# Performance work log

Hardware: AMD Instinct MI355X
Metric: run time of the kernel (lower is better)

The kernel has to match this reference:

```python
import jax, jax.numpy as jnp
import numpy as np

B, N, K, IN_CH = 512, 64, 16, 6   # graphs, nodes per graph, knn, input features
EPS = 1e-5


def _w(key, shape, fan_in):
    return jax.random.normal(key, shape, jnp.float32) / np.sqrt(fan_in)


def setup_inputs() -> dict:
    key = jax.random.key(0)
    ks = jax.random.split(key, 16)
    f32 = jnp.float32
    inp = {
        "x": jax.random.normal(ks[0], (B * N, IN_CH), f32),
        "batch": (jnp.arange(B * N, dtype=jnp.int32) // N).astype(jnp.int32),
        # input projection 6 -> 64
        "w_in": _w(ks[1], (IN_CH, 64), IN_CH), "g_in": jnp.ones(64, f32), "b_in": jnp.zeros(64, f32),
        # ec1: SharedMLP([128, 64, 64])
        "w1a": _w(ks[2], (128, 64), 128), "g1a": jnp.ones(64, f32), "b1a": jnp.zeros(64, f32),
        "w1b": _w(ks[3], (64, 64), 64),   "g1b": jnp.ones(64, f32), "b1b": jnp.zeros(64, f32),
        # ec2: SharedMLP([128, 128, 128])
        "w2a": _w(ks[4], (128, 128), 128), "g2a": jnp.ones(128, f32), "b2a": jnp.zeros(128, f32),
        "w2b": _w(ks[5], (128, 128), 128), "g2b": jnp.ones(128, f32), "b2b": jnp.zeros(128, f32),
        # ec3: SharedMLP([256, 256, 256])
        "w3a": _w(ks[6], (256, 256), 256), "g3a": jnp.ones(256, f32), "b3a": jnp.zeros(256, f32),
        "w3b": _w(ks[7], (256, 256), 256), "g3b": jnp.ones(256, f32), "b3b": jnp.zeros(256, f32),
        # classifier head (dropout is identity in eval mode)
        "wc1": _w(ks[8], (896, 512), 896), "gc1": jnp.ones(512, f32), "bc1": jnp.zeros(512, f32),
        "wc2": _w(ks[9], (512, 256), 512), "gc2": jnp.ones(256, f32), "bc2": jnp.zeros(256, f32),
        "wc3": _w(ks[10], (256, 2), 256),  "bc3": jnp.zeros(2, f32),
    }
    return inp


def bn(h, g, b):
    # training-mode BatchNorm1d over all leading (node/edge) dims, biased var
    ax = tuple(range(h.ndim - 1))
    m = h.mean(ax)
    v = h.var(ax)
    return g * (h - m) * jax.lax.rsqrt(v + EPS) + b


def lrelu(h):
    return jax.nn.leaky_relu(h, 0.2)


def knn(x):
    # x: [B,N,C]; per-graph squared-Euclidean kNN (excluding self)
    sq = jnp.sum(x * x, -1)
    d = sq[:, :, None] - 2.0 * jnp.einsum('bnc,bmc->bnm', x, x) + sq[:, None, :]
    _, idx = jax.lax.top_k(-d, K + 1)  # K+1 smallest distances
    return idx[:, :, 1:]               # drop self -> [B,N,K]


def edge_conv(x, w1, g1, b1, w2, g2, b2):
    # Dynamic EdgeConv, aggr='max'. Edge (src=centre c, dst=neighbour n):
    # target x_i = x_n, message = MLP(cat[x_i, x_j - x_i]) with x_j = x_c.
    idx = knn(x)                                     # [B,N,K]
    xn = jax.vmap(lambda xb, ib: xb[ib])(x, idx)     # [B,N,K,C] neighbours
    xc = x[:, :, None, :]                            # centres broadcast
    feat = jnp.concatenate([xn, xc - xn], -1)        # [B,N,K,2C]
    h = lrelu(bn(feat @ w1, g1, b1))
    h = lrelu(bn(h @ w2, g2, b2))                    # [B,N,K,Cout]
    C = h.shape[-1]

    def scatter_max(ib, hb):  # per-graph max-scatter to destination nodes
        out = jnp.full((N, C), -jnp.inf, hb.dtype)
        return out.at[ib.reshape(-1)].max(hb.reshape(-1, C))

    res = jax.vmap(scatter_max)(idx, h)
    return jnp.where(jnp.isneginf(res), 0.0, res)    # nodes w/o in-edges -> 0


def reference(x, batch, w_in, g_in, b_in,
              w1a, g1a, b1a, w1b, g1b, b1b,
              w2a, g2a, b2a, w2b, g2b, b2b,
              w3a, g3a, b3a, w3b, g3b, b3b,
              wc1, gc1, bc1, wc2, gc2, bc2, wc3, bc3):
    # batch == arange(B*N)//N (equal-size graphs), encoded by the [B,N] reshape
    h0 = lrelu(bn(x @ w_in, g_in, b_in)).reshape(B, N, 64)
    h1 = edge_conv(h0, w1a, g1a, b1a, w1b, g1b, b1b)   # [B,N,64]
    h2 = edge_conv(h1, w2a, g2a, b2a, w2b, g2b, b2b)   # [B,N,128]
    h3 = edge_conv(h2, w3a, g3a, b3a, w3b, g3b, b3b)   # [B,N,256]
    h = jnp.concatenate([h1, h2, h3], -1)              # [B,N,448]
    pooled = jnp.concatenate([h.mean(1), h.max(1)], -1)  # [B,896]
    z = lrelu(bn(pooled @ wc1, gc1, bc1))
    z = lrelu(bn(z @ wc2, gc2, bc2))
    return z @ wc3 + bc3                               # [B,2] logits
```

## Files before the change

### kernel.cpp

```cpp
#include <hip/hip_runtime.h>
#include <hip/hip_fp16.h>
#include <math.h>

#define BB 512
#define NN 64
#define KNB 16
#define NPTS (BB*NN)
#define NEDGE (BB*NN*KNB)
#define EPSV 1e-5f

typedef __attribute__((ext_vector_type(8))) _Float16 f16x8;
typedef __attribute__((ext_vector_type(4))) _Float16 f16x4;
typedef __attribute__((ext_vector_type(4))) float f32x4;

__device__ __forceinline__ float lrelu(float x){ return fmaxf(x, 0.2f*x); }
__device__ __forceinline__ unsigned encf(float f){
    unsigned u = __float_as_uint(f);
    return (u & 0x80000000u) ? ~u : (u | 0x80000000u);
}
__device__ __forceinline__ float decf(unsigned e){
    unsigned u = (e & 0x80000000u) ? (e ^ 0x80000000u) : ~e;
    return __uint_as_float(u);
}
#define ENC_NEGINF 0x007FFFFFu

__device__ __forceinline__ void split2h(float v, _Float16& h, _Float16& m){
    h = (_Float16)v;
    float r = v - (float)h;
    m = (_Float16)(r * 2048.0f);
}

__global__ void k_input(const float* __restrict__ x, const float* __restrict__ w,
                        float* __restrict__ h0){
    __shared__ float wls[6*64];
    int t = threadIdx.x;
    for (int i = t; i < 6*64; i += 256) wls[i] = w[i];
    __syncthreads();
    int row = blockIdx.x*256 + t;
    float xv[6];
#pragma unroll
    for (int k = 0; k < 6; k++) xv[k] = x[row*6 + k];
#pragma unroll 8
    for (int c = 0; c < 64; c++){
        float acc = 0.f;
#pragma unroll
        for (int k = 0; k < 6; k++) acc += xv[k]*wls[k*64 + c];
        h0[(size_t)row*64 + c] = acc;
    }
}

__global__ void k_colstats_part(const float* __restrict__ h,
                                float* __restrict__ pS, float* __restrict__ pQ){
    int t = threadIdx.x;
    int c = t & 63;
    int g = t >> 6;
    int p = blockIdx.x*4 + g;
    const int rpb = NPTS/256;
    int r0 = p*rpb;
    float s = 0.f, q = 0.f;
    for (int r = r0; r < r0 + rpb; r++){
        float v = h[(size_t)r*64 + c];
        s += v; q += v*v;
    }
    pS[c*256 + p] = s;
    pQ[c*256 + p] = q;
}

__global__ void k_bnfin_part(const float* __restrict__ pS, const float* __restrict__ pQ,
                             const float* __restrict__ g, const float* __restrict__ b,
                             float* __restrict__ cA, float* __restrict__ cB,
                             int P, float invM){
    int c = threadIdx.x;
    const float* ps = pS + (size_t)c*P;
    const float* pq = pQ + (size_t)c*P;
    float s = 0.f, q = 0.f;
    for (int p = 0; p < P; p += 4){
        float4 vs = *(const float4*)(ps + p);
        float4 vq = *(const float4*)(pq + p);
        s += vs.x + vs.y + vs.z + vs.w;
        q += vq.x + vq.y + vq.z + vq.w;
    }
    float m = s*invM;
    float v = q*invM - m*m;
    v = v < 0.f ? 0.f : v;
    float a = g[c]*rsqrtf(v + EPSV);
    cA[c] = a;
    cB[c] = b[c] - m*a;
}

__global__ void k_bnfin(const float* gs, const float* gq, const float* g,
                        const float* b, float* cA, float* cB, int C, float invM){
    int c = blockIdx.x*blockDim.x + threadIdx.x;
    if (c < C){
        float m = gs[c]*invM;
        float v = gq[c]*invM - m*m;
        v = v < 0.f ? 0.f : v;
        float a = g[c]*rsqrtf(v + EPSV);
        cA[c] = a;
        cB[c] = b[c] - m*a;
    }
}

__global__ void k_apply(float* h, const float* __restrict__ cA,
                        const float* __restrict__ cB, int C, int total){
    int i = blockIdx.x*256 + threadIdx.x;
    if (i < total){
        int c = i & (C-1);
        h[i] = lrelu(cA[c]*h[i] + cB[c]);
    }
}

template<int C>
__global__ void k_knn(const float* __restrict__ x, int* __restrict__ idxg){
    const int CP = C + 4;
    __shared__ __align__(16) float xls[64*CP];
    __shared__ float sq[64];
    __shared__ __align__(16) float dls[64*64];
    int t = threadIdx.x, b = blockIdx.x;
    const float* xb = x + (size_t)b*64*C;
    for (int i = t; i < 64*C; i += 256){
        int n = i / C, c = i & (C-1);
        xls[n*CP + c] = xb[i];
    }
    __syncthreads();
    if (t < 64){
        float s = 0.f;
        for (int c = 0; c < C; c += 4){
            float4 v = *(const float4*)&xls[t*CP + c];
            s += v.x*v.x + v.y*v.y + v.z*v.z + v.w*v.w;
        }
        sq[t] = s;
    }
    __syncthreads();
    {
        int n  = t >> 2;
        int m0 = (t & 3)*16;
        float acc[16];
#pragma unroll
        for (int i = 0; i < 16; i++) acc[i] = 0.f;
        const float* an = &xls[n*CP];
        const float* bm = &xls[m0*CP];
        for (int c = 0; c < C; c += 4){
            float4 a = *(const float4*)(an + c);
#pragma unroll
            for (int i = 0; i < 16; i++){
                float4 bv = *(const float4*)(bm + i*CP + c);
                acc[i] += a.x*bv.x + a.y*bv.y + a.z*bv.z + a.w*bv.w;
            }
        }
        float sn = sq[n];
#pragma unroll
        for (int i4 = 0; i4 < 16; i4 += 4){
            float4 dv;
            dv.x = sn - 2.0f*acc[i4+0] + sq[m0+i4+0];
            dv.y = sn - 2.0f*acc[i4+1] + sq[m0+i4+1];
            dv.z = sn - 2.0f*acc[i4+2] + sq[m0+i4+2];
            dv.w = sn - 2.0f*acc[i4+3] + sq[m0+i4+3];
            *(float4*)&dls[n*64 + m0 + i4] = dv;
        }
    }
    __syncthreads();
    int lane = t & 63, w = t >> 6;
    for (int pr = 0; pr < 16; pr += 4){
        int n0 = w*16 + pr;
        unsigned long long c0 = (((unsigned long long)encf(dls[(n0+0)*64 + lane])) << 32) | (unsigned)lane;
        unsigned long long c1 = (((unsigned long long)encf(dls[(n0+1)*64 + lane])) << 32) | (unsigned)lane;
        unsigned long long c2 = (((unsigned long long)encf(dls[(n0+2)*64 + lane])) << 32) | (unsigned)lane;
        unsigned long long c3 = (((unsigned long long)encf(dls[(n0+3)*64 + lane])) << 32) | (unsigned)lane;
#pragma unroll
        for (int k = 2; k <= 64; k <<= 1){
#pragma unroll
            for (int j = k >> 1; j > 0; j >>= 1){
                bool keepmin = ((lane & j) == 0) == ((lane & k) == 0);
                unsigned long long o0 = __shfl_xor(c0, j, 64);
                unsigned long long o1 = __shfl_xor(c1, j, 64);
                unsigned long long o2 = __shfl_xor(c2, j, 64);
                unsigned long long o3 = __shfl_xor(c3, j, 64);
                c0 = keepmin ? (c0 < o0 ? c0 : o0) : (c0 < o0 ? o0 : c0);
                c1 = keepmin ? (c1 < o1 ? c1 : o1) : (c1 < o1 ? o1 : c1);
                c2 = keepmin ? (c2 < o2 ? c2 : o2) : (c2 < o2 ? o2 : c2);
                c3 = keepmin ? (c3 < o3 ? c3 : o3) : (c3 < o3 ? o3 : c3);
            }
        }
        if (lane >= 1 && lane <= KNB){
            int base = b*1024 + n0*16 + lane - 1;
            idxg[base]      = (int)(c0 & 0xffffffffu);
            idxg[base + 16] = (int)(c1 & 0xffffffffu);
            idxg[base + 32] = (int)(c2 & 0xffffffffu);
            idxg[base + 48] = (int)(c3 & 0xffffffffu);
        }
    }
}

__global__ void k_wprep_all(const float* __restrict__ w1a, const float* __restrict__ w2a,
                            const float* __restrict__ w3a,
                            _Float16* __restrict__ w1bh, _Float16* __restrict__ w1bm,
                            _Float16* __restrict__ w1dh, _Float16* __restrict__ w1dm,
                            _Float16* __restrict__ w2bh, _Float16* __restrict__ w2bm,
                            _Float16* __restrict__ w2dh, _Float16* __restrict__ w2dm,
                            _Float16* __restrict__ w3bh, _Float16* __restrict__ w3dh){
    int blk = blockIdx.x, t = threadIdx.x;
    if (blk < 16){
        const int CIN = 64, CMID = 64;
        int i = blk*256 + t;
        int k = i / CMID, c = i - k*CMID;
        float wb = w1a[(size_t)(CIN + k)*CMID + c];
        float wd = w1a[(size_t)k*CMID + c] - wb;
        size_t o = (size_t)c*CIN + k;
        _Float16 h, m;
        split2h(wb, h, m); w1bh[o] = h; w1bm[o] = m;
        split2h(wd, h, m); w1dh[o] = h; w1dm[o] = m;
    } else if (blk < 48){
        const int CIN = 64, CMID = 128;
        int i = (blk - 16)*256 + t;
        int k = i / CMID, c = i - k*CMID;
        float wb = w2a[(size_t)(CIN + k)*CMID + c];
        float wd = w2a[(size_t)k*CMID + c] - wb;
        size_t o = (size_t)c*CIN + k;
        _Float16 h, m;
        split2h(wb, h, m); w2bh[o] = h; w2bm[o] = m;
        split2h(wd, h, m); w2dh[o] = h; w2dm[o] = m;
    } else {
        const int CIN = 128, CMID = 256;
        int i = (blk - 48)*256 + t;
        int k = i / CMID, c = i - k*CMID;
        float wb = w3a[(size_t)(CIN + k)*CMID + c];
        float wd = w3a[(size_t)k*CMID + c] - wb;
        size_t o = (size_t)c*CIN + k;
        w3bh[o] = (_Float16)wb;
        w3dh[o] = (_Float16)wd;
    }
}

template<int CIN, int CMID>
__global__ __launch_bounds__(256)
void k_mm1x(const float* __restrict__ x,
            const _Float16* __restrict__ wbh, const _Float16* __restrict__ wbm,
            const _Float16* __restrict__ wdh, const _Float16* __restrict__ wdm,
            float* __restrict__ P, float* __restrict__ Q){
    int t = threadIdx.x, b = blockIdx.x;
    int lane = t & 63, w = t >> 6;
    int lrow = lane & 15, lk = lane >> 4;
    const int KT = CIN/32;
    f16x8 ah[KT], am[KT];
    {
        const float* xr = x + ((size_t)b*64 + w*16 + lrow)*CIN;
#pragma unroll
        for (int kt = 0; kt < KT; kt++){
            union { f16x8 v; _Float16 u[8]; } H, M;
#pragma unroll
            for (int j = 0; j < 8; j++)
                split2h(xr[kt*32 + lk*8 + j], H.u[j], M.u[j]);
            ah[kt] = H.v; am[kt] = M.v;
        }
    }
#pragma unroll
    for (int ct = 0; ct < CMID/16; ct++){
        int col = ct*16 + lrow;
        f32x4 aPM = {0,0,0,0}, aPC = {0,0,0,0};
        f32x4 aQM = {0,0,0,0}, aQC = {0,0,0,0};
#pragma unroll
        for (int kt = 0; kt < KT; kt++){
            size_t bo = (size_t)col*CIN + kt*32 + lk*8;
            f16x8 bbh = *(const f16x8*)(wbh + bo);
            f16x8 bbm = *(const f16x8*)(wbm + bo);
            f16x8 bdh = *(const f16x8*)(wdh + bo);
            f16x8 bdm = *(const f16x8*)(wdm + bo);
            aPM = __builtin_amdgcn_mfma_f32_16x16x32_f16(ah[kt], bbh, aPM, 0, 0, 0);
            aPC = __builtin_amdgcn_mfma_f32_16x16x32_f16(ah[kt], bbm, aPC, 0, 0, 0);
            aPC = __builtin_amdgcn_mfma_f32_16x16x32_f16(am[kt], bbh, aPC, 0, 0, 0);
            aQM = __builtin_amdgcn_mfma_f32_16x16x32_f16(ah[kt], bdh, aQM, 0, 0, 0);
            aQC = __builtin_amdgcn_mfma_f32_16x16x32_f16(ah[kt], bdm, aQC, 0, 0, 0);
            aQC = __builtin_amdgcn_mfma_f32_16x16x32_f16(am[kt], bdh, aQC, 0, 0, 0);
        }
#pragma unroll
        for (int u = 0; u < 4; u++){
            size_t o = ((size_t)b*64 + w*16 + lk*4 + u)*CMID + col;
            P[o] = aPM[u] + aPC[u]*(1.0f/2048.0f);
            Q[o] = aQM[u] + aQC[u]*(1.0f/2048.0f);
        }
    }
}

template<int CIN, int CMID>
__global__ __launch_bounds__(256)
void k_mm1xh(const float* __restrict__ x,
             const _Float16* __restrict__ wbh, const _Float16* __restrict__ wdh,
             _Float16* __restrict__ P, _Float16* __restrict__ Q){
    int t = threadIdx.x, b = blockIdx.x;
    int lane = t & 63, w = t >> 6;
    int lrow = lane & 15, lk = lane >> 4;
    const int KT = CIN/32;
    f16x8 ah[KT];
    {
        const float* xr = x + ((size_t)b*64 + w*16 + lrow)*CIN;
#pragma unroll
        for (int kt = 0; kt < KT; kt++){
            union { f16x8 v; _Float16 u[8]; } H;
#pragma unroll
            for (int j = 0; j < 8; j++)
                H.u[j] = (_Float16)xr[kt*32 + lk*8 + j];
            ah[kt] = H.v;
        }
    }
#pragma unroll
    for (int ct = 0; ct < CMID/16; ct++){
        int col = ct*16 + lrow;
        f32x4 aP = {0,0,0,0}, aQ = {0,0,0,0};
#pragma unroll
        for (int kt = 0; kt < KT; kt++){
            size_t bo = (size_t)col*CIN + kt*32 + lk*8;
            f16x8 bbh = *(const f16x8*)(wbh + bo);
            f16x8 bdh = *(const f16x8*)(wdh + bo);
            aP = __builtin_amdgcn_mfma_f32_16x16x32_f16(ah[kt], bbh, aP, 0, 0, 0);
            aQ = __builtin_amdgcn_mfma_f32_16x16x32_f16(ah[kt], bdh, aQ, 0, 0, 0);
        }
#pragma unroll
        for (int u = 0; u < 4; u++){
            size_t o = ((size_t)b*64 + w*16 + lk*4 + u)*CMID + col;
            P[o] = (_Float16)aP[u];
            Q[o] = (_Float16)aQ[u];
        }
    }
}

template<int CMID>
__global__ void k_stats1p(const float* __restrict__ P, const float* __restrict__ Q,
                          const int* __restrict__ idxg,
                          float* __restrict__ pS, float* __restrict__ pQ){
    int t = threadIdx.x, b = blockIdx.x;
    const int NG = 256/CMID;
    const int PT = 512*NG;
    int c = t & (CMID-1);
    int g = t / CMID;
    int epg = 1024/NG;
    const float* Pb = P + (size_t)b*64*CMID;
    const float* Qb = Q + (size_t)b*64*CMID;
    const int* ib = idxg + b*1024;
    float s = 0.f, q = 0.f;
    for (int e = g*epg; e < (g+1)*epg; e++){
        int n = e >> 4;
        int j = ib[e];
        float v = Pb[n*CMID + c] + Qb[j*CMID + c];
        s += v; q += v*v;
    }
    int p = b*NG + g;
    pS[(size_t)c*PT + p] = s;
    pQ[(size_t)c*PT + p] = q;
}

__global__ void k_stats1h(const _Float16* __restrict__ P, const _Float16* __restrict__ Q,
                          const int* __restrict__ idxg,
                          float* __restrict__ pS, float* __restrict__ pQ){
    __shared__ int ils[1024];
    int t = threadIdx.x, b = blockIdx.x;
    for (int i = t; i < 1024; i += 256) ils[i] = idxg[b*1024 + i];
    __syncthreads();
    const _Float16* Pb = P + (size_t)b*64*256;
    const _Float16* Qb = Q + (size_t)b*64*256;
    float s = 0.f, q = 0.f;
    for (int n = 0; n < 64; n++){
        float p = (float)Pb[n*256 + t];
#pragma unroll 4
        for (int k = 0; k < 16; k++){
            int j = ils[n*16 + k];
            float v = p + (float)Qb[j*256 + t];
            s += v; q += v*v;
        }
    }
    pS[(size_t)t*512 + b] = s;
    pQ[(size_t)t*512 + b] = q;
}

template<int CMID, int COUT, int NSET>
__global__ __launch_bounds__(256, 3)
void k_mm2s(const float* __restrict__ P, const float* __restrict__ Q,
            const int* __restrict__ idxg,
            const float* __restrict__ cA1, const float* __restrict__ cB1,
            const float* __restrict__ w2, const float* __restrict__ g2,
            unsigned* __restrict__ outenc,
            float* __restrict__ pS, float* __restrict__ pQ){
    const int AS = CMID + 8;
    const int NCOL = 64*NSET;
    const int NM = CMID/32;
    __shared__ __align__(16) _Float16 act_h[32*AS];
    __shared__ __align__(16) _Float16 act_m[32*AS];
    __shared__ unsigned maxtab[NCOL*65];
    __shared__ __align__(4) unsigned char ils8[1024];
    int t = threadIdx.x, b = blockIdx.x, cc = blockIdx.y;
    int lane = t & 63, w = t >> 6;
    int lrow = lane & 15, lk = lane >> 4;

    for (int i = t; i < 1024; i += 256) ils8[i] = (unsigned char)idxg[b*1024 + i];
    for (int i = t; i < NCOL*65; i += 256) maxtab[i] = ENC_NEGINF;

    int kq  = (t*4) & (CMID-1);
    int le0 = (t*4) / CMID;
    int PH  = (le0*NM) >> 4;
    float4 caq = *(const float4*)(cA1 + kq);
    float4 cbq = *(const float4*)(cB1 + kq);

    const int KT = CMID/32;
    f16x8 bh[NSET][KT], bm[NSET][KT];
    float sg[NSET];
    int ccBase = cc*NCOL;
#pragma unroll
    for (int s = 0; s < NSET; s++){
        int ncol = ccBase + s*64 + w*16 + lrow;
#pragma unroll
        for (int kt = 0; kt < KT; kt++){
            union { f16x8 v; _Float16 u[8]; } uh, um;
#pragma unroll
            for (int j = 0; j < 8; j++){
                int k = kt*32 + lk*8 + j;
                split2h(w2[(size_t)k*COUT + ncol], uh.u[j], um.u[j]);
            }
            bh[s][kt] = uh.v; bm[s][kt] = um.v;
        }
        sg[s] = (g2[ncol] < 0.0f) ? -1.0f : 1.0f;
    }
    float ss[NSET], qq[NSET];
#pragma unroll
    for (int s = 0; s < NSET; s++){ ss[s] = 0.f; qq[s] = 0.f; }
    const float* Pb = P + (size_t)b*64*CMID;
    const float* Qb = Q + (size_t)b*64*CMID;
    __syncthreads();

    unsigned jw;
    if (NM == 4) jw = *(const unsigned*)&ils8[le0*4];
    else         jw = *(const unsigned short*)&ils8[le0*2];
    float4 pv = *(const float4*)(Pb + PH*CMID + kq);
    float4 qvr[NM];
#pragma unroll
    for (int m = 0; m < NM; m++)
        qvr[m] = *(const float4*)(Qb + (size_t)((jw >> (8*m)) & 0xffu)*CMID + kq);

    for (int ch = 0; ch < 32; ch++){
#pragma unroll
        for (int m = 0; m < NM; m++){
            int le = le0*NM + m;
            float4 qv = qvr[m];
            float v0 = lrelu(caq.x*(pv.x + qv.x) + cbq.x);
            float v1 = lrelu(caq.y*(pv.y + qv.y) + cbq.y);
            float v2 = lrelu(caq.z*(pv.z + qv.z) + cbq.z);
            float v3 = lrelu(caq.w*(pv.w + qv.w) + cbq.w);
            union { f16x4 v; _Float16 u[4]; } hh, mm;
            split2h(v0, hh.u[0], mm.u[0]);
            split2h(v1, hh.u[1], mm.u[1]);
            split2h(v2, hh.u[2], mm.u[2]);
            split2h(v3, hh.u[3], mm.u[3]);
            *(f16x4*)&act_h[le*AS + kq] = hh.v;
            *(f16x4*)&act_m[le*AS + kq] = mm.v;
        }
        __syncthreads();

        if (ch < 31){
            if (NM == 4) jw = *(const unsigned*)&ils8[(ch+1)*32 + le0*4];
            else         jw = *(const unsigned short*)&ils8[(ch+1)*32 + le0*2];
            pv = *(const float4*)(Pb + (2*(ch+1) + PH)*CMID + kq);
#pragma unroll
            for (int m = 0; m < NM; m++)
                qvr[m] = *(const float4*)(Qb + (size_t)((jw >> (8*m)) & 0xffu)*CMID + kq);
        }
        int jj[2][4];
#pragma unroll
        for (int r = 0; r < 2; r++){
            unsigned wrd = *(const unsigned*)&ils8[ch*32 + r*16 + lk*4];
#pragma unroll
            for (int u = 0; u < 4; u++)
                jj[r][u] = (int)((wrd >> (8*u)) & 0xffu);
        }

        f32x4 accM[2][NSET], accC[2][NSET];
#pragma unroll
        for (int r = 0; r < 2; r++)
#pragma unroll
            for (int s = 0; s < NSET; s++){
                accM[r][s] = {0.f,0.f,0.f,0.f};
                accC[r][s] = {0.f,0.f,0.f,0.f};
            }
#pragma unroll
        for (int kt = 0; kt < KT; kt++){
            int ko = kt*32 + lk*8;
#pragma unroll
            for (int r = 0; r < 2; r++){
                f16x8 ah = *(const f16x8*)&act_h[(r*16 + lrow)*AS + ko];
                f16x8 am = *(const f16x8*)&act_m[(r*16 + lrow)*AS + ko];
#pragma unroll
                for (int s = 0; s < NSET; s++){
                    accM[r][s] = __builtin_amdgcn_mfma_f32_16x16x32_f16(ah, bh[s][kt], accM[r][s], 0, 0, 0);
                    accC[r][s] = __builtin_amdgcn_mfma_f32_16x16x32_f16(ah, bm[s][kt], accC[r][s], 0, 0, 0);
                    accC[r][s] = __builtin_amdgcn_mfma_f32_16x16x32_f16(am, bh[s][kt], accC[r][s], 0, 0, 0);
                }
            }
        }
#pragma unroll
        for (int r = 0; r < 2; r++){
#pragma unroll
            for (int s = 0; s < NSET; s++){
#pragma unroll
                for (int u = 0; u < 4; u++){
                    float v = accM[r][s][u] + accC[r][s][u]*(1.0f/2048.0f);
                    ss[s] += v; qq[s] += v*v;
                    int colL = s*64 + w*16 + lrow;
                    atomicMax(&maxtab[colL*65 + jj[r][u]], encf(sg[s]*v));
                }
            }
        }
        __syncthreads();
    }
#pragma unroll
    for (int s = 0; s < NSET; s++){
        ss[s] += __shfl_xor(ss[s], 16, 64); ss[s] += __shfl_xor(ss[s], 32, 64);
        qq[s] += __shfl_xor(qq[s], 16, 64); qq[s] += __shfl_xor(qq[s], 32, 64);
        if (lane < 16){
            pS[(size_t)(ccBase + s*64 + w*16 + lane)*512 + b] = ss[s];
            pQ[(size_t)(ccBase + s*64 + w*16 + lane)*512 + b] = qq[s];
        }
    }
    for (int i = t; i < 64*NCOL; i += 256){
        int colL = i % NCOL, j = i / NCOL;
        outenc[((size_t)b*64 + j)*COUT + ccBase + colL] = maxtab[colL*65 + j];
    }
}

template<int CMID, int COUT, int NSET>
__global__ __launch_bounds__(256, 3)
void k_mm2xh(const _Float16* __restrict__ P, const _Float16* __restrict__ Q,
             const int* __restrict__ idxg,
             const float* __restrict__ cA1, const float* __restrict__ cB1,
             const float* __restrict__ w2, const float* __restrict__ g2,
             unsigned* __restrict__ outenc,
             float* __restrict__ pS, float* __restrict__ pQ){
    const int AS = CMID + 8;
    const int NCOL = 64*NSET;
    const int NM = CMID/64;
    __shared__ __align__(16) _Float16 act[32*AS];
    __shared__ unsigned maxtab[NCOL*65];
    __shared__ __align__(4) unsigned char ils8[1024];
    int t = threadIdx.x, b = blockIdx.x, cc = blockIdx.y;
    int lane = t & 63, w = t >> 6;
    int lrow = lane & 15, lk = lane >> 4;

    for (int i = t; i < 1024; i += 256) ils8[i] = (unsigned char)idxg[b*1024 + i];
    for (int i = t; i < NCOL*65; i += 256) maxtab[i] = ENC_NEGINF;

    int kq  = (t*8) & (CMID-1);
    int le0 = (t*8) / CMID;
    int PH  = (le0*NM) >> 4;
    union { f16x8 v; _Float16 u[8]; } cah, cbh;
#pragma unroll
    for (int j = 0; j < 8; j++){
        cah.u[j] = (_Float16)cA1[kq + j];
        cbh.u[j] = (_Float16)cB1[kq + j];
    }

    const int KT = CMID/32;
    f16x8 breg[NSET][KT];
    float sg[NSET];
    int ccBase = cc*NCOL;
#pragma unroll
    for (int s = 0; s < NSET; s++){
        int ncol = ccBase + s*64 + w*16 + lrow;
#pragma unroll
        for (int kt = 0; kt < KT; kt++){
            union { f16x8 v; _Float16 u[8]; } bu;
#pragma unroll
            for (int j = 0; j < 8; j++){
                int k = kt*32 + lk*8 + j;
                bu.u[j] = (_Float16)w2[(size_t)k*COUT + ncol];
            }
            breg[s][kt] = bu.v;
        }
        sg[s] = (g2[ncol] < 0.0f) ? -1.0f : 1.0f;
    }
    float ss[NSET], qq[NSET];
#pragma unroll
    for (int s = 0; s < NSET; s++){ ss[s] = 0.f; qq[s] = 0.f; }
    const _Float16* Pb = P + (size_t)b*64*CMID;
    const _Float16* Qb = Q + (size_t)b*64*CMID;
    __syncthreads();

    unsigned jw = *(const unsigned*)&ils8[le0*4];
    f16x8 pv = *(const f16x8*)(Pb + (size_t)PH*CMID + kq);
    f16x8 qvr[NM];
#pragma unroll
    for (int m = 0; m < NM; m++)
        qvr[m] = *(const f16x8*)(Qb + (size_t)((jw >> (8*m)) & 0xffu)*CMID + kq);

    for (int ch = 0; ch < 32; ch++){
#pragma unroll
        for (int m = 0; m < NM; m++){
            int le = le0*NM + m;
            f16x8 v = cah.v*(pv + qvr[m]) + cbh.v;
            f16x8 vm = v * (_Float16)0.2f;
#if __has_builtin(__builtin_elementwise_max)
            *(f16x8*)&act[le*AS + kq] = __builtin_elementwise_max(v, vm);
#else
            union { f16x8 x; _Float16 e8[8]; } V, M, R;
            V.x = v; M.x = vm;
#pragma unroll
            for (int u = 0; u < 8; u++)
                R.e8[u] = (V.e8[u] > (_Float16)0.0f) ? V.e8[u] : M.e8[u];
            *(f16x8*)&act[le*AS + kq] = R.x;
#endif
        }
        __syncthreads();

        if (ch < 31){
            jw = *(const unsigned*)&ils8[(ch+1)*32 + le0*4];
            pv = *(const f16x8*)(Pb + (size_t)(2*(ch+1) + PH)*CMID + kq);
#pragma unroll
            for (int m = 0; m < NM; m++)
                qvr[m] = *(const f16x8*)(Qb + (size_t)((jw >> (8*m)) & 0xffu)*CMID + kq);
        }
        int jj[2][4];
#pragma unroll
        for (int r = 0; r < 2; r++){
            unsigned wrd = *(const unsigned*)&ils8[ch*32 + r*16 + lk*4];
#pragma unroll
            for (int u = 0; u < 4; u++)
                jj[r][u] = (int)((wrd >> (8*u)) & 0xffu);
        }

        f32x4 acc[2][NSET];
#pragma unroll
        for (int r = 0; r < 2; r++)
#pragma unroll
            for (int s = 0; s < NSET; s++) acc[r][s] = {0.f,0.f,0.f,0.f};
#pragma unroll
        for (int kt = 0; kt < KT; kt++){
            int ko = kt*32 + lk*8;
#pragma unroll
            for (int r = 0; r < 2; r++){
                f16x8 a = *(const f16x8*)&act[(r*16 + lrow)*AS + ko];
#pragma unroll
                for (int s = 0; s < NSET; s++)
                    acc[r][s] = __builtin_amdgcn_mfma_f32_16x16x32_f16(a, breg[s][kt], acc[r][s], 0, 0, 0);
            }
        }
#pragma unroll
        for (int r = 0; r < 2; r++){
#pragma unroll
            for (int s = 0; s < NSET; s++){
#pragma unroll
                for (int u = 0; u < 4; u++){
                    float v = acc[r][s][u];
                    ss[s] += v; qq[s] += v*v;
                    int colL = s*64 + w*16 + lrow;
                    atomicMax(&maxtab[colL*65 + jj[r][u]], encf(sg[s]*v));
                }
            }
        }
        __syncthreads();
    }
#pragma unroll
    for (int s = 0; s < NSET; s++){
        ss[s] += __shfl_xor(ss[s], 16, 64); ss[s] += __shfl_xor(ss[s], 32, 64);
        qq[s] += __shfl_xor(qq[s], 16, 64); qq[s] += __shfl_xor(qq[s], 32, 64);
        if (lane < 16){
            pS[(size_t)(ccBase + s*64 + w*16 + lane)*512 + b] = ss[s];
            pQ[(size_t)(ccBase + s*64 + w*16 + lane)*512 + b] = qq[s];
        }
    }
    for (int i = t; i < 64*NCOL; i += 256){
        int colL = i % NCOL, j = i / NCOL;
        outenc[((size_t)b*64 + j)*COUT + ccBase + colL] = maxtab[colL*65 + j];
    }
}

__global__ void k_final_ec(unsigned* __restrict__ buf, const float* __restrict__ cA,
                           const float* __restrict__ cB, const float* __restrict__ g,
                           int C, int total){
    int i = blockIdx.x*256 + threadIdx.x;
    if (i >= total) return;
    int c = i & (C-1);
    unsigned e = buf[i];
    float r;
    if (e == ENC_NEGINF) r = 0.0f;
    else {
        float s = (g[c] < 0.0f) ? -1.0f : 1.0f;
        float v = s*decf(e);
        r = lrelu(cA[c]*v + cB[c]);
    }
    ((float*)buf)[i] = r;
}

__global__ void k_pool(const float* __restrict__ h1, const float* __restrict__ h2,
                       const unsigned* __restrict__ h3e,
                       const float* __restrict__ cA3, const float* __restrict__ cB3,
                       const float* __restrict__ g3, float* __restrict__ pooled){
    int t = threadIdx.x, b = blockIdx.x;
    for (int c = t; c < 448; c += 256){
        float s = 0.f, mx = -INFINITY;
        if (c < 192){
            const float* src; int C, cl;
            if (c < 64){ src = h1; C = 64;  cl = c; }
            else { src = h2; C = 128; cl = c - 64; }
            const float* p = src + (size_t)b*64*C + cl;
            for (int n = 0; n < 64; n++){
                float v = p[(size_t)n*C];
                s += v; mx = fmaxf(mx, v);
            }
        } else {
            int cl = c - 192;
            float ca = cA3[cl], cb = cB3[cl];
            float sgn = (g3[cl] < 0.0f) ? -1.0f : 1.0f;
            const unsigned* p = h3e + (size_t)b*64*256 + cl;
            for (int n = 0; n < 64; n++){
                unsigned e = p[(size_t)n*256];
                float v;
                if (e == ENC_NEGINF) v = 0.0f;
                else v = lrelu(ca*(sgn*decf(e)) + cb);
                s += v; mx = fmaxf(mx, v);
            }
        }
        pooled[b*896 + c] = s*(1.0f/64.0f);
        pooled[b*896 + 448 + c] = mx;
    }
}

__global__ void k_fc1(const float* __restrict__ pooled, const float* __restrict__ w,
                      float* __restrict__ z, float* gs, float* gq){
    int r = blockIdx.x;
    int co = blockIdx.y*256 + threadIdx.x;
    const float* pr = pooled + r*896;
    float acc = 0.f;
    for (int k = 0; k < 896; k++) acc += pr[k]*w[(size_t)k*512 + co];
    z[(size_t)r*512 + co] = acc;
    atomicAdd(&gs[co], acc);
    atomicAdd(&gq[co], acc*acc);
}

__global__ void k_fc2(const float* __restrict__ z1, const float* __restrict__ cA,
                      const float* __restrict__ cB, const float* __restrict__ w,
                      float* __restrict__ z2, float* gs, float* gq){
    int r = blockIdx.x;
    int co = threadIdx.x;
    const float* zr = z1 + (size_t)r*512;
    float acc = 0.f;
    for (int k = 0; k < 512; k++){
        float v = lrelu(cA[k]*zr[k] + cB[k]);
        acc += v*w[(size_t)k*256 + co];
    }
    z2[(size_t)r*256 + co] = acc;
    atomicAdd(&gs[co], acc);
    atomicAdd(&gq[co], acc*acc);
}

__global__ void k_fc3(const float* __restrict__ z2, const float* __restrict__ cA,
                      const float* __restrict__ cB, const float* __restrict__ w,
                      const float* __restrict__ bias, float* __restrict__ out){
    int r = blockIdx.x*256 + threadIdx.x;
    const float* zr = z2 + (size_t)r*256;
    float a0 = 0.f, a1 = 0.f;
    for (int k = 0; k < 256; k++){
        float v = lrelu(cA[k]*zr[k] + cB[k]);
        a0 += v*w[k*2 + 0];
        a1 += v*w[k*2 + 1];
    }
    out[r*2 + 0] = a0 + bias[0];
    out[r*2 + 1] = a1 + bias[1];
}

extern "C" void kernel_launch(void* const* d_in, const int* in_sizes, int n_in,
                              void* d_out, int out_size, void* d_ws, size_t ws_size,
                              hipStream_t stream){
    const float* x    = (const float*)d_in[0];
    const float* w_in = (const float*)d_in[2];
    const float* g_in = (const float*)d_in[3];
    const float* b_in = (const float*)d_in[4];
    const float* w1a  = (const float*)d_in[5];
    const float* g1a  = (const float*)d_in[6];
    const float* b1a  = (const float*)d_in[7];
    const float* w1b  = (const float*)d_in[8];
    const float* g1b  = (const float*)d_in[9];
    const float* b1b  = (const float*)d_in[10];
    const float* w2a  = (const float*)d_in[11];
    const float* g2a  = (const float*)d_in[12];
    const float* b2a  = (const float*)d_in[13];
    const float* w2b  = (const float*)d_in[14];
    const float* g2b  = (const float*)d_in[15];
    const float* b2b  = (const float*)d_in[16];
    const float* w3a  = (const float*)d_in[17];
    const float* g3a  = (const float*)d_in[18];
    const float* b3a  = (const float*)d_in[19];
    const float* w3b  = (const float*)d_in[20];
    const float* g3b  = (const float*)d_in[21];
    const float* b3b  = (const float*)d_in[22];
    const float* wc1  = (const float*)d_in[23];
    const float* gc1  = (const float*)d_in[24];
    const float* bc1  = (const float*)d_in[25];
    const float* wc2  = (const float*)d_in[26];
    const float* gc2  = (const float*)d_in[27];
    const float* bc2  = (const float*)d_in[28];
    const float* wc3  = (const float*)d_in[29];
    const float* bc3  = (const float*)d_in[30];

    char* ws = (char*)d_ws;
    size_t off = 0;
    auto alloc = [&](size_t bytes){
        size_t o = off; off = (off + bytes + 255) & ~(size_t)255; return o;
    };
    float* h0     = (float*)(ws + alloc((size_t)NPTS*64*4));
    float* h1     = (float*)(ws + alloc((size_t)NPTS*64*4));
    float* h2     = (float*)(ws + alloc((size_t)NPTS*128*4));
    float* h3     = (float*)(ws + alloc((size_t)NPTS*256*4));
    float* P      = (float*)(ws + alloc((size_t)NPTS*256*4));
    float* Q      = (float*)(ws + alloc((size_t)NPTS*256*4));
    int*   idx    = (int*)  (ws + alloc((size_t)NPTS*16*4));
    float* pooled = (float*)(ws + alloc((size_t)512*896*4));
    float* z1     = (float*)(ws + alloc((size_t)512*512*4));
    float* z2     = (float*)(ws + alloc((size_t)512*256*4));
    float* pS     = (float*)(ws + alloc((size_t)131072*4));
    float* pQ     = (float*)(ws + alloc((size_t)131072*4));
    float* stats  = (float*)(ws + alloc((size_t)2048*4));
    float* coefs  = (float*)(ws + alloc((size_t)3456*4));
    _Float16* wsp = (_Float16*)(ws + alloc((size_t)114688*2));

    _Float16 *w1bh = wsp,          *w1bm = wsp+4096,
             *w1dh = wsp+8192,     *w1dm = wsp+12288;
    _Float16 *w2bh = wsp+16384,    *w2bm = wsp+24576,
             *w2dh = wsp+32768,    *w2dm = wsp+40960;
    _Float16 *w3bh = wsp+49152,    *w3dh = wsp+81920;

    float *f1s  = stats,       *f1q  = stats+512;
    float *f2s  = stats+1024,  *f2q  = stats+1280;
    float *cA0   = coefs,      *cB0   = coefs+64;
    float *cA1a  = coefs+128,  *cB1a  = coefs+192;
    float *cA1b  = coefs+256,  *cB1b  = coefs+320;
    float *cA2a  = coefs+384,  *cB2a  = coefs+512;
    float *cA2b  = coefs+640,  *cB2b  = coefs+768;
    float *cA3a  = coefs+896,  *cB3a  = coefs+1152;
    float *cA3b  = coefs+1408, *cB3b  = coefs+1664;
    float *cAf1  = coefs+1920, *cBf1  = coefs+2432;
    float *cAf2  = coefs+2944, *cBf2  = coefs+3200;

    (void)hipMemsetAsync(stats, 0, 2048*4, stream);

    k_wprep_all<<<176, 256, 0, stream>>>(w1a, w2a, w3a,
                                         w1bh, w1bm, w1dh, w1dm,
                                         w2bh, w2bm, w2dh, w2dm,
                                         w3bh, w3dh);

    k_input<<<NPTS/256, 256, 0, stream>>>(x, w_in, h0);
    k_colstats_part<<<64, 256, 0, stream>>>(h0, pS, pQ);
    k_bnfin_part<<<1, 64, 0, stream>>>(pS, pQ, g_in, b_in, cA0, cB0, 256, 1.0f/NPTS);
    k_apply<<<(NPTS*64)/256, 256, 0, stream>>>(h0, cA0, cB0, 64, NPTS*64);

    k_knn<64><<<BB, 256, 0, stream>>>(h0, idx);
    k_mm1x<64,64><<<BB, 256, 0, stream>>>(h0, w1bh, w1bm, w1dh, w1dm, P, Q);
    k_stats1p<64><<<BB, 256, 0, stream>>>(P, Q, idx, pS, pQ);
    k_bnfin_part<<<1, 64, 0, stream>>>(pS, pQ, g1a, b1a, cA1a, cB1a, 2048, 1.0f/NEDGE);
    k_mm2s<64,64,1><<<dim3(BB,1), 256, 0, stream>>>(P, Q, idx, cA1a, cB1a, w1b, g1b,
                                                    (unsigned*)h1, pS, pQ);
    k_bnfin_part<<<1, 64, 0, stream>>>(pS, pQ, g1b, b1b, cA1b, cB1b, 512, 1.0f/NEDGE);
    k_final_ec<<<(NPTS*64)/256, 256, 0, stream>>>((unsigned*)h1, cA1b, cB1b, g1b, 64, NPTS*64);

    k_knn<64><<<BB, 256, 0, stream>>>(h1, idx);
    k_mm1x<64,128><<<BB, 256, 0, stream>>>(h1, w2bh, w2bm, w2dh, w2dm, P, Q);
    k_stats1p<128><<<BB, 256, 0, stream>>>(P, Q, idx, pS, pQ);
    k_bnfin_part<<<1, 128, 0, stream>>>(pS, pQ, g2a, b2a, cA2a, cB2a, 1024, 1.0f/NEDGE);
    k_mm2s<128,128,2><<<dim3(BB,1), 256, 0, stream>>>(P, Q, idx, cA2a, cB2a, w2b, g2b,
                                                      (unsigned*)h2, pS, pQ);
    k_bnfin_part<<<1, 128, 0, stream>>>(pS, pQ, g2b, b2b, cA2b, cB2b, 512, 1.0f/NEDGE);
    k_final_ec<<<(NPTS*128)/256, 256, 0, stream>>>((unsigned*)h2, cA2b, cB2b, g2b, 128, NPTS*128);

    k_knn<128><<<BB, 256, 0, stream>>>(h2, idx);
    k_mm1xh<128,256><<<BB, 256, 0, stream>>>(h2, w3bh, w3dh, (_Float16*)P, (_Float16*)Q);
    k_stats1h<<<BB, 256, 0, stream>>>((_Float16*)P, (_Float16*)Q, idx, pS, pQ);
    k_bnfin_part<<<1, 256, 0, stream>>>(pS, pQ, g3a, b3a, cA3a, cB3a, 512, 1.0f/NEDGE);
    k_mm2xh<256,256,2><<<dim3(BB,2), 256, 0, stream>>>((_Float16*)P, (_Float16*)Q, idx,
                                                       cA3a, cB3a, w3b, g3b,
                                                       (unsigned*)h3, pS, pQ);
    k_bnfin_part<<<1, 256, 0, stream>>>(pS, pQ, g3b, b3b, cA3b, cB3b, 512, 1.0f/NEDGE);

    k_pool<<<BB, 256, 0, stream>>>(h1, h2, (const unsigned*)h3, cA3b, cB3b, g3b, pooled);
    k_fc1<<<dim3(512,2), 256, 0, stream>>>(pooled, wc1, z1, f1s, f1q);
    k_bnfin<<<2, 256, 0, stream>>>(f1s, f1q, gc1, bc1, cAf1, cBf1, 512, 1.0f/512);
    k_fc2<<<512, 256, 0, stream>>>(z1, cAf1, cBf1, wc2, z2, f2s, f2q);
    k_bnfin<<<1, 256, 0, stream>>>(f2s, f2q, gc2, bc2, cAf2, cBf2, 256, 1.0f/512);
    k_fc3<<<2, 256, 0, stream>>>(z2, cAf2, cBf2, wc3, bc3, (float*)d_out);

    (void)in_sizes; (void)n_in; (void)out_size; (void)ws_size;
}
```

Measured before the change: 1.139 ms.

## Fuse BN-apply and decode into consumers; fold edge stats into first matmul

Removes the standalone BN-apply and final edge-conv decode passes. Consumers (knn, first-layer matmul, pool) now apply the BN affine, leaky ReLU and max-encoding decode on the fly as they read. The per-edge BN statistics kernels are folded into the first edge-conv matmul: P and Q tiles are staged in shared memory and reduced using the neighbour indices. This cuts several launches and full-tensor global round trips, at the cost of repeated decode work in multiple consumers and higher LDS use per block.

```diff
diff --git a/kernel.cpp b/kernel.cpp
--- a/kernel.cpp
+++ b/kernel.cpp
@@ -23,6 +23,12 @@
     return __uint_as_float(u);
 }
 #define ENC_NEGINF 0x007FFFFFu
+
+__device__ __forceinline__ float dec_ec(unsigned e, float ca, float cb, float gv){
+    if (e == ENC_NEGINF) return 0.0f;
+    float s = (gv < 0.0f) ? -1.0f : 1.0f;
+    return lrelu(ca*(s*decf(e)) + cb);
+}
 
 __device__ __forceinline__ void split2h(float v, _Float16& h, _Float16& m){
     h = (_Float16)v;
@@ -101,26 +107,27 @@
     }
 }
 
-__global__ void k_apply(float* h, const float* __restrict__ cA,
-                        const float* __restrict__ cB, int C, int total){
-    int i = blockIdx.x*256 + threadIdx.x;
-    if (i < total){
-        int c = i & (C-1);
-        h[i] = lrelu(cA[c]*h[i] + cB[c]);
-    }
-}
-
-template<int C>
-__global__ void k_knn(const float* __restrict__ x, int* __restrict__ idxg){
+template<int C, int MODE>
+__global__ void k_knn(const void* __restrict__ xin, int* __restrict__ idxg,
+                      const float* __restrict__ cA, const float* __restrict__ cB,
+                      const float* __restrict__ g){
     const int CP = C + 4;
     __shared__ __align__(16) float xls[64*CP];
     __shared__ float sq[64];
     __shared__ __align__(16) float dls[64*64];
     int t = threadIdx.x, b = blockIdx.x;
-    const float* xb = x + (size_t)b*64*C;
-    for (int i = t; i < 64*C; i += 256){
-        int n = i / C, c = i & (C-1);
-        xls[n*CP + c] = xb[i];
+    if (MODE == 0){
+        const float* xb = (const float*)xin + (size_t)b*64*C;
+        for (int i = t; i < 64*C; i += 256){
+            int n = i / C, c = i & (C-1);
+            xls[n*CP + c] = lrelu(cA[c]*xb[i] + cB[c]);
+        }
+    } else {
+        const unsigned* xb = (const unsigned*)xin + (size_t)b*64*C;
+        for (int i = t; i < 64*C; i += 256){
+            int n = i / C, c = i & (C-1);
+            xls[n*CP + c] = dec_ec(xb[i], cA[c], cB[c], g[c]);
+        }
     }
     __syncthreads();
     if (t < 64){
@@ -232,25 +239,45 @@
     }
 }
 
-template<int CIN, int CMID>
+template<int CIN, int CMID, int MODE>
 __global__ __launch_bounds__(256)
-void k_mm1x(const float* __restrict__ x,
-            const _Float16* __restrict__ wbh, const _Float16* __restrict__ wbm,
-            const _Float16* __restrict__ wdh, const _Float16* __restrict__ wdm,
-            float* __restrict__ P, float* __restrict__ Q){
+void k_mm1x_st(const void* __restrict__ xin,
+               const float* __restrict__ cAin, const float* __restrict__ cBin,
+               const float* __restrict__ gin,
+               const _Float16* __restrict__ wbh, const _Float16* __restrict__ wbm,
+               const _Float16* __restrict__ wdh, const _Float16* __restrict__ wdm,
+               const int* __restrict__ idxg,
+               float* __restrict__ P, float* __restrict__ Q,
+               float* __restrict__ pS, float* __restrict__ pQ){
+    const int ASP = CMID + 9;
+    __shared__ float Pls[64*ASP];
+    __shared__ float Qls[64*ASP];
+    __shared__ int ils[1024];
     int t = threadIdx.x, b = blockIdx.x;
     int lane = t & 63, w = t >> 6;
     int lrow = lane & 15, lk = lane >> 4;
+    for (int i = t; i < 1024; i += 256) ils[i] = idxg[b*1024 + i];
+
     const int KT = CIN/32;
     f16x8 ah[KT], am[KT];
     {
-        const float* xr = x + ((size_t)b*64 + w*16 + lrow)*CIN;
+        size_t rowg = (size_t)b*64 + w*16 + lrow;
 #pragma unroll
         for (int kt = 0; kt < KT; kt++){
             union { f16x8 v; _Float16 u[8]; } H, M;
 #pragma unroll
-            for (int j = 0; j < 8; j++)
-                split2h(xr[kt*32 + lk*8 + j], H.u[j], M.u[j]);
+            for (int j = 0; j < 8; j++){
+                int k = kt*32 + lk*8 + j;
+                float v;
+                if (MODE == 0){
+                    float raw = ((const float*)xin)[rowg*CIN + k];
+                    v = lrelu(cAin[k]*raw + cBin[k]);
+                } else {
+                    unsigned e = ((const unsigned*)xin)[rowg*CIN + k];
+                    v = dec_ec(e, cAin[k], cBin[k], gin[k]);
+                }
+                split2h(v, H.u[j], M.u[j]);
+            }
             ah[kt] = H.v; am[kt] = M.v;
         }
     }
@@ -275,31 +302,66 @@
         }
 #pragma unroll
         for (int u = 0; u < 4; u++){
-            size_t o = ((size_t)b*64 + w*16 + lk*4 + u)*CMID + col;
-            P[o] = aPM[u] + aPC[u]*(1.0f/2048.0f);
-            Q[o] = aQM[u] + aQC[u]*(1.0f/2048.0f);
-        }
+            int row = w*16 + lk*4 + u;
+            size_t o = ((size_t)b*64 + row)*CMID + col;
+            float pv = aPM[u] + aPC[u]*(1.0f/2048.0f);
+            float qv = aQM[u] + aQC[u]*(1.0f/2048.0f);
+            P[o] = pv; Q[o] = qv;
+            Pls[row*ASP + col] = pv;
+            Qls[row*ASP + col] = qv;
+        }
+    }
+    __syncthreads();
+    {
+        const int NG = 256/CMID;
+        const int PT = 512*NG;
+        int c  = t & (CMID-1);
+        int gg = t / CMID;
+        int epg = 1024/NG;
+        float s = 0.f, q = 0.f;
+        for (int e = gg*epg; e < (gg+1)*epg; e++){
+            int n = e >> 4;
+            int j = ils[e];
+            float v = Pls[n*ASP + c] + Qls[j*ASP + c];
+            s += v; q += v*v;
+        }
+        int p = b*NG + gg;
+        pS[(size_t)c*PT + p] = s;
+        pQ[(size_t)c*PT + p] = q;
     }
 }
 
 template<int CIN, int CMID>
 __global__ __launch_bounds__(256)
-void k_mm1xh(const float* __restrict__ x,
-             const _Float16* __restrict__ wbh, const _Float16* __restrict__ wdh,
-             _Float16* __restrict__ P, _Float16* __restrict__ Q){
+void k_mm1xh_st(const unsigned* __restrict__ xin,
+                const float* __restrict__ cAin, const float* __restrict__ cBin,
+                const float* __restrict__ gin,
+                const _Float16* __restrict__ wbh, const _Float16* __restrict__ wdh,
+                const int* __restrict__ idxg,
+                _Float16* __restrict__ P, _Float16* __restrict__ Q,
+                float* __restrict__ pS, float* __restrict__ pQ){
+    const int ASP = CMID + 9;
+    __shared__ _Float16 Pls[64*ASP];
+    __shared__ _Float16 Qls[64*ASP];
+    __shared__ int ils[1024];
     int t = threadIdx.x, b = blockIdx.x;
     int lane = t & 63, w = t >> 6;
     int lrow = lane & 15, lk = lane >> 4;
+    for (int i = t; i < 1024; i += 256) ils[i] = idxg[b*1024 + i];
+
     const int KT = CIN/32;
     f16x8 ah[KT];
     {
-        const float* xr = x + ((size_t)b*64 + w*16 + lrow)*CIN;
+        size_t rowg = (size_t)b*64 + w*16 + lrow;
 #pragma unroll
         for (int kt = 0; kt < KT; kt++){
             union { f16x8 v; _Float16 u[8]; } H;
 #pragma unroll
-            for (int j = 0; j < 8; j++)
-                H.u[j] = (_Float16)xr[kt*32 + lk*8 + j];
+            for (int j = 0; j < 8; j++){
+                int k = kt*32 + lk*8 + j;
+                unsigned e = xin[rowg*CIN + k];
+                H.u[j] = (_Float16)dec_ec(e, cAin[k], cBin[k], gin[k]);
+            }
             ah[kt] = H.v;
         }
     }
@@ -317,59 +379,30 @@
         }
 #pragma unroll
         for (int u = 0; u < 4; u++){
-            size_t o = ((size_t)b*64 + w*16 + lk*4 + u)*CMID + col;
-            P[o] = (_Float16)aP[u];
-            Q[o] = (_Float16)aQ[u];
-        }
-    }
-}
-
-template<int CMID>
-__global__ void k_stats1p(const float* __restrict__ P, const float* __restrict__ Q,
-                          const int* __restrict__ idxg,
-                          float* __restrict__ pS, float* __restrict__ pQ){
-    int t = threadIdx.x, b = blockIdx.x;
-    const int NG = 256/CMID;
-    const int PT = 512*NG;
-    int c = t & (CMID-1);
-    int g = t / CMID;
-    int epg = 1024/NG;
-    const float* Pb = P + (size_t)b*64*CMID;
-    const float* Qb = Q + (size_t)b*64*CMID;
-    const int* ib = idxg + b*1024;
-    float s = 0.f, q = 0.f;
-    for (int e = g*epg; e < (g+1)*epg; e++){
-        int n = e >> 4;
-        int j = ib[e];
-        float v = Pb[n*CMID + c] + Qb[j*CMID + c];
-        s += v; q += v*v;
-    }
-    int p = b*NG + g;
-    pS[(size_t)c*PT + p] = s;
-    pQ[(size_t)c*PT + p] = q;
-}
-
-__global__ void k_stats1h(const _Float16* __restrict__ P, const _Float16* __restrict__ Q,
-                          const int* __restrict__ idxg,
-                          float* __restrict__ pS, float* __restrict__ pQ){
-    __shared__ int ils[1024];
-    int t = threadIdx.x, b = blockIdx.x;
-    for (int i = t; i < 1024; i += 256) ils[i] = idxg[b*1024 + i];
+            int row = w*16 + lk*4 + u;
+            size_t o = ((size_t)b*64 + row)*CMID + col;
+            _Float16 hp = (_Float16)aP[u];
+            _Float16 hq = (_Float16)aQ[u];
+            P[o] = hp; Q[o] = hq;
+            Pls[row*ASP + col] = hp;
+            Qls[row*ASP + col] = hq;
+        }
+    }
     __syncthreads();
-    const _Float16* Pb = P + (size_t)b*64*256;
-    const _Float16* Qb = Q + (size_t)b*64*256;
-    float s = 0.f, q = 0.f;
-    for (int n = 0; n < 64; n++){
-        float p = (float)Pb[n*256 + t];
+    {
+        float s = 0.f, q = 0.f;
+        for (int n = 0; n < 64; n++){
+            float p = (float)Pls[n*ASP + t];
 #pragma unroll 4
-        for (int k = 0; k < 16; k++){
-            int j = ils[n*16 + k];
-            float v = p + (float)Qb[j*256 + t];
-            s += v; q += v*v;
-        }
-    }
-    pS[(size_t)t*512 + b] = s;
-    pQ[(size_t)t*512 + b] = q;
+            for (int k = 0; k < 16; k++){
+                int j = ils[n*16 + k];
+                float v = p + (float)Qls[j*ASP + t];
+                s += v; q += v*v;
+            }
+        }
+        pS[(size_t)t*512 + b] = s;
+        pQ[(size_t)t*512 + b] = q;
+    }
 }
 
 template<int CMID, int COUT, int NSET>
@@ -669,51 +702,25 @@
     }
 }
 
-__global__ void k_final_ec(unsigned* __restrict__ buf, const float* __restrict__ cA,
-                           const float* __restrict__ cB, const float* __restrict__ g,
-                           int C, int total){
-    int i = blockIdx.x*256 + threadIdx.x;
-    if (i >= total) return;
-    int c = i & (C-1);
-    unsigned e = buf[i];
-    float r;
-    if (e == ENC_NEGINF) r = 0.0f;
-    else {
-        float s = (g[c] < 0.0f) ? -1.0f : 1.0f;
-        float v = s*decf(e);
-        r = lrelu(cA[c]*v + cB[c]);
-    }
-    ((float*)buf)[i] = r;
-}
-
-__global__ void k_pool(const float* __restrict__ h1, const float* __restrict__ h2,
+__global__ void k_pool(const unsigned* __restrict__ h1e, const unsigned* __restrict__ h2e,
                        const unsigned* __restrict__ h3e,
+                       const float* __restrict__ cA1, const float* __restrict__ cB1,
+                       const float* __restrict__ g1,
+                       const float* __restrict__ cA2, const float* __restrict__ cB2,
+                       const float* __restrict__ g2,
                        const float* __restrict__ cA3, const float* __restrict__ cB3,
-                       const float* __restrict__ g3, float* __restrict__ pooled){
+                       const float* __restrict__ g3,
+                       float* __restrict__ pooled){
     int t = threadIdx.x, b = blockIdx.x;
     for (int c = t; c < 448; c += 256){
+        const unsigned* p; int C; float ca, cb, gv;
+        if (c < 64){        p = h1e + (size_t)b*64*64  + c;        C = 64;  ca = cA1[c];     cb = cB1[c];     gv = g1[c]; }
+        else if (c < 192){  p = h2e + (size_t)b*64*128 + (c-64);   C = 128; ca = cA2[c-64];  cb = cB2[c-64];  gv = g2[c-64]; }
+        else {              p = h3e + (size_t)b*64*256 + (c-192);  C = 256; ca = cA3[c-192]; cb = cB3[c-192]; gv = g3[c-192]; }
         float s = 0.f, mx = -INFINITY;
-        if (c < 192){
-            const float* src; int C, cl;
-            if (c < 64){ src = h1; C = 64;  cl = c; }
-            else { src = h2; C = 128; cl = c - 64; }
-            const float* p = src + (size_t)b*64*C + cl;
-            for (int n = 0; n < 64; n++){
-                float v = p[(size_t)n*C];
-                s += v; mx = fmaxf(mx, v);
-            }
-        } else {
-            int cl = c - 192;
-            float ca = cA3[cl], cb = cB3[cl];
-            float sgn = (g3[cl] < 0.0f) ? -1.0f : 1.0f;
-            const unsigned* p = h3e + (size_t)b*64*256 + cl;
-            for (int n = 0; n < 64; n++){
-                unsigned e = p[(size_t)n*256];
-                float v;
-                if (e == ENC_NEGINF) v = 0.0f;
-                else v = lrelu(ca*(sgn*decf(e)) + cb);
-                s += v; mx = fmaxf(mx, v);
-            }
+        for (int n = 0; n < 64; n++){
+            float v = dec_ec(p[(size_t)n*C], ca, cb, gv);
+            s += v; mx = fmaxf(mx, v);
         }
         pooled[b*896 + c] = s*(1.0f/64.0f);
         pooled[b*896 + 448 + c] = mx;
@@ -846,36 +853,39 @@
     k_input<<<NPTS/256, 256, 0, stream>>>(x, w_in, h0);
     k_colstats_part<<<64, 256, 0, stream>>>(h0, pS, pQ);
     k_bnfin_part<<<1, 64, 0, stream>>>(pS, pQ, g_in, b_in, cA0, cB0, 256, 1.0f/NPTS);
-    k_apply<<<(NPTS*64)/256, 256, 0, stream>>>(h0, cA0, cB0, 64, NPTS*64);
-
-    k_knn<64><<<BB, 256, 0, stream>>>(h0, idx);
-    k_mm1x<64,64><<<BB, 256, 0, stream>>>(h0, w1bh, w1bm, w1dh, w1dm, P, Q);
-    k_stats1p<64><<<BB, 256, 0, stream>>>(P, Q, idx, pS, pQ);
+
+    k_knn<64,0><<<BB, 256, 0, stream>>>(h0, idx, cA0, cB0, nullptr);
+    k_mm1x_st<64,64,0><<<BB, 256, 0, stream>>>(h0, cA0, cB0, nullptr,
+                                               w1bh, w1bm, w1dh, w1dm, idx,
+                                               P, Q, pS, pQ);
     k_bnfin_part<<<1, 64, 0, stream>>>(pS, pQ, g1a, b1a, cA1a, cB1a, 2048, 1.0f/NEDGE);
     k_mm2s<64,64,1><<<dim3(BB,1), 256, 0, stream>>>(P, Q, idx, cA1a, cB1a, w1b, g1b,
                                                     (unsigned*)h1, pS, pQ);
     k_bnfin_part<<<1, 64, 0, stream>>>(pS, pQ, g1b, b1b, cA1b, cB1b, 512, 1.0f/NEDGE);
-    k_final_ec<<<(NPTS*64)/256, 256, 0, stream>>>((unsigned*)h1, cA1b, cB1b, g1b, 64, NPTS*64);
-
-    k_knn<64><<<BB, 256, 0, stream>>>(h1, idx);
-    k_mm1x<64,128><<<BB, 256, 0, stream>>>(h1, w2bh, w2bm, w2dh, w2dm, P, Q);
-    k_stats1p<128><<<BB, 256, 0, stream>>>(P, Q, idx, pS, pQ);
+
+    k_knn<64,1><<<BB, 256, 0, stream>>>(h1, idx, cA1b, cB1b, g1b);
+    k_mm1x_st<64,128,1><<<BB, 256, 0, stream>>>(h1, cA1b, cB1b, g1b,
+                                                w2bh, w2bm, w2dh, w2dm, idx,
+                                                P, Q, pS, pQ);
     k_bnfin_part<<<1, 128, 0, stream>>>(pS, pQ, g2a, b2a, cA2a, cB2a, 1024, 1.0f/NEDGE);
     k_mm2s<128,128,2><<<dim3(BB,1), 256, 0, stream>>>(P, Q, idx, cA2a, cB2a, w2b, g2b,
                                                       (unsigned*)h2, pS, pQ);
     k_bnfin_part<<<1, 128, 0, stream>>>(pS, pQ, g2b, b2b, cA2b, cB2b, 512, 1.0f/NEDGE);
-    k_final_ec<<<(NPTS*128)/256, 256, 0, stream>>>((unsigned*)h2, cA2b, cB2b, g2b, 128, NPTS*128);
-
-    k_knn<128><<<BB, 256, 0, stream>>>(h2, idx);
-    k_mm1xh<128,256><<<BB, 256, 0, stream>>>(h2, w3bh, w3dh, (_Float16*)P, (_Float16*)Q);
-    k_stats1h<<<BB, 256, 0, stream>>>((_Float16*)P, (_Float16*)Q, idx, pS, pQ);
+
+    k_knn<128,1><<<BB, 256, 0, stream>>>(h2, idx, cA2b, cB2b, g2b);
+    k_mm1xh_st<128,256><<<BB, 256, 0, stream>>>((const unsigned*)h2, cA2b, cB2b, g2b,
+                                                w3bh, w3dh, idx,
+                                                (_Float16*)P, (_Float16*)Q, pS, pQ);
     k_bnfin_part<<<1, 256, 0, stream>>>(pS, pQ, g3a, b3a, cA3a, cB3a, 512, 1.0f/NEDGE);
     k_mm2xh<256,256,2><<<dim3(BB,2), 256, 0, stream>>>((_Float16*)P, (_Float16*)Q, idx,
                                                        cA3a, cB3a, w3b, g3b,
                                                        (unsigned*)h3, pS, pQ);
     k_bnfin_part<<<1, 256, 0, stream>>>(pS, pQ, g3b, b3b, cA3b, cB3b, 512, 1.0f/NEDGE);
 
-    k_pool<<<BB, 256, 0, stream>>>(h1, h2, (const unsigned*)h3, cA3b, cB3b, g3b, pooled);
+    k_pool<<<BB, 256, 0, stream>>>((const unsigned*)h1, (const unsigned*)h2,
+                                   (const unsigned*)h3,
+                                   cA1b, cB1b, g1b, cA2b, cB2b, g2b, cA3b, cB3b, g3b,
+                                   pooled);
     k_fc1<<<dim3(512,2), 256, 0, stream>>>(pooled, wc1, z1, f1s, f1q);
     k_bnfin<<<2, 256, 0, stream>>>(f1s, f1q, gc1, bc1, cAf1, cBf1, 512, 1.0f/512);
     k_fc2<<<512, 256, 0, stream>>>(z1, cAf1, cBf1, wc2, z2, f2s, f2q);
```

Result: faster. 1.107 ms (-2.8%).
